# Kernel optimization log

Hardware: AMD Instinct MI355X
Metric: run time of the kernel (lower is better)

The kernel has to match this reference:

```python
import jax, jax.numpy as jnp
import numpy as np

B, NP, DIM = 32, 1369, 768
NCLS, K = 200, 5
C = NCLS + 1          # n_classes + background
H = W = 37            # sqrt(NP)
GAMMA = 0.99
SCALE = 4.0
SINKHORN_ITERS = 3
PCA_ITERS = 10
PCA_THRESH = 0.5
EPS = 1e-8


def _l2norm(x):
    return x / jnp.clip(jnp.linalg.norm(x, axis=-1, keepdims=True), EPS)


def setup_inputs() -> dict:
    key = jax.random.key(0)
    k1, k2, k3 = jax.random.split(key, 3)
    patch_tokens = jax.random.normal(k1, (B, NP, DIM), dtype=jnp.float32)
    labels = jax.random.randint(k2, (B,), 0, NCLS)
    prototypes = 0.02 * jax.random.normal(k3, (C, K, DIM), dtype=jnp.float32)  # trunc_normal std=0.02 approx
    sa = jnp.full((NCLS, K), 0.5, dtype=jnp.float32)
    scale = jnp.asarray(SCALE, dtype=jnp.float32)
    return {"patch_tokens": patch_tokens, "labels": labels,
            "prototypes": prototypes, "sa": sa, "scale": scale}


def reference(patch_tokens, labels, prototypes, sa, scale):
    # --- cosine patch-prototype similarity ---
    tok_n = _l2norm(patch_tokens)                 # [B, NP, D]
    pro_n = _l2norm(prototypes)                   # [C, K, D]
    logits = scale * jnp.einsum('bnd,ckd->bnck', tok_n, pro_n)  # [B, NP, C, K]

    # --- avg pooling + 'sa' classification head ---
    image_logits = logits.mean(axis=1)            # [B, C, K]
    sa_w = jax.nn.softmax(sa, axis=-1) * K        # [NCLS, K]
    class_logits = (image_logits[:, :NCLS, :] * sa_w).sum(axis=-1)  # [B, NCLS]

    # --- PCA pseudo patch labels (power iteration, q=1, centered) ---
    X = jax.lax.stop_gradient(patch_tokens).reshape(-1, DIM)  # [N, D]
    Xc = X - X.mean(axis=0, keepdims=True)
    v = jax.random.normal(jax.random.key(42), (DIM,), dtype=jnp.float32)
    for _ in range(PCA_ITERS):
        u = Xc @ v
        v = Xc.T @ u
        v = v / jnp.clip(jnp.linalg.norm(v), EPS)
    u = Xc @ v
    U = u / jnp.clip(jnp.linalg.norm(u), EPS)     # leading left singular vector
    U_scaled = (U - U.min()) / jnp.clip(U.max() - U.min(), EPS)
    U_img = U_scaled.reshape(B, H, W)
    pseudo = jnp.where(U_img <= PCA_THRESH,
                       labels[:, None, None],
                       C - 1).astype(jnp.int32)   # [B, H, W]

    # --- online clustering: masked sinkhorn vectorized over classes ---
    flat_lab = pseudo.reshape(-1)                 # [N]
    cls_ids = jnp.arange(C)
    mask = (flat_lab[:, None] == cls_ids[None, :]).astype(jnp.float32)  # [N, C]
    Nc = mask.sum(axis=0)                         # [C] fg patch count per class
    Lf = jax.lax.stop_gradient(logits).reshape(-1, C, K)
    Q = jnp.exp(Lf) * mask[:, :, None]            # [N, C, K], zero outside class mask
    Q = Q / jnp.clip(Q.sum(axis=(0, 2)), EPS)[None, :, None]
    Ncc = jnp.clip(Nc, 1.0)
    for _ in range(SINKHORN_ITERS):
        Q = Q / jnp.clip(Q.sum(axis=0), EPS)[None] / K           # col normalize
        Q = Q / jnp.clip(Q.sum(axis=2, keepdims=True), EPS) / Ncc[None, :, None]  # row normalize
    Q = Q * Nc[None, :, None]
    tok_flat = jax.lax.stop_gradient(tok_n).reshape(-1, DIM)
    P_new = jnp.einsum('nck,nd->ckd', Q, tok_flat)               # [C, K, D]
    updated = GAMMA * prototypes + (1.0 - GAMMA) * P_new          # momentum update
    present = jnp.isin(cls_ids, labels)                           # classes in this batch
    new_prototypes = jnp.where(present[:, None, None], updated, prototypes)

    return (logits, image_logits, class_logits, pseudo, new_prototypes)
```

## Files before the change

### kernel.cpp

```cpp
#include <hip/hip_runtime.h>

constexpr int   BB    = 32;
constexpr int   NPP   = 1369;
constexpr int   DIMC  = 768;
constexpr int   NCLSC = 200;
constexpr int   KP    = 5;
constexpr int   CC    = 201;
constexpr int   CKC   = 1005;
constexpr int   NPAD  = 1024;
constexpr int   NTOK  = BB * NPP;
constexpr float EPSF  = 1e-8f;
constexpr int   PWIN  = 128;
constexpr int   MTILES = 343;
constexpr int   NSLAB = 4;

typedef __attribute__((ext_vector_type(8))) short bf16x8;
typedef __attribute__((ext_vector_type(4))) float f32x4;

constexpr size_t O_LOG = 0;
constexpr size_t O_IMG = (size_t)NTOK * CKC;
constexpr size_t O_CLS = O_IMG + (size_t)BB * CKC;
constexpr size_t O_PSE = O_CLS + (size_t)BB * NCLSC;
constexpr size_t O_PRO = O_PSE + (size_t)NTOK;

constexpr size_t W_PRONBF = 0;
constexpr size_t W_INVN   = W_PRONBF + (size_t)NPAD*DIMC/2;
constexpr size_t W_MU     = W_INVN + NTOK;
constexpr size_t W_COLS   = W_MU + 2*DIMC;
constexpr size_t W_VBUF   = W_COLS + 2*NSLAB*DIMC;
constexpr size_t W_SSUM   = W_VBUF + 2*11*NSLAB*DIMC;
constexpr size_t W_TSUM   = W_SSUM + 128;
constexpr size_t W_NC     = W_TSUM + CC;
constexpr size_t W_FILL   = W_NC + CC;
constexpr size_t W_PRES   = W_FILL + CC;
constexpr size_t ZG_LEN   = (W_PRES + CC) - W_COLS;
constexpr size_t W_CSQ    = W_PRES + CC;
constexpr size_t W_U      = ((W_CSQ + CKC) + 1) & ~(size_t)1;
constexpr size_t W_PART   = W_U + 2*NTOK;
constexpr size_t W_SCAL   = W_PART + 2*1536;
constexpr size_t W_Q      = W_SCAL + 16;
constexpr size_t W_PNEW   = W_Q + (size_t)NTOK*KP;
constexpr size_t W_PLAB   = W_PNEW + (size_t)CC*KP*DIMC;
constexpr size_t W_OFFS   = W_PLAB + NTOK;
constexpr size_t W_RLST   = W_OFFS + 256;
constexpr size_t W_XBF    = ((W_RLST + NTOK) + 3) & ~(size_t)3;
constexpr size_t W_END_BIG  = W_XBF + (size_t)(NTOK + 128)*DIMC/2;
constexpr size_t W_PRON32   = W_XBF;
constexpr size_t W_END_FALL = W_PRON32 + (size_t)CKC*DIMC;

__device__ __forceinline__ unsigned short f2bf(float x) {
    unsigned u = __float_as_uint(x);
    unsigned r = (u + 0x7fffu + ((u >> 16) & 1u)) >> 16;
    return (unsigned short)r;
}
__device__ __forceinline__ float bf2f(unsigned short h) {
    return __uint_as_float(((unsigned)h) << 16);
}

typedef __attribute__((address_space(3))) unsigned int as3_u32;
typedef __attribute__((address_space(1))) unsigned int as1_u32;
__device__ __forceinline__ void gload16(const unsigned short* g, unsigned short* l) {
    __builtin_amdgcn_global_load_lds((as1_u32*)g, (as3_u32*)l, 16, 0, 0);
}

__global__ void fill_zero(float* p, int n) {
    int i = blockIdx.x * 256 + threadIdx.x;
    if (i < n) p[i] = 0.0f;
}

__global__ __launch_bounds__(256) void tok_stats(const float* __restrict__ X,
                                                 float* __restrict__ invn,
                                                 double* __restrict__ colsD,
                                                 unsigned short* __restrict__ xbf) {
    __shared__ double csh[4][768];
    const int tid  = threadIdx.x;
    const int lane = tid & 63;
    const int wid  = tid >> 6;
    const int gw   = blockIdx.x * 4 + wid;
    double cacc[3][4];
    #pragma unroll
    for (int j = 0; j < 3; j++)
        #pragma unroll
        for (int t = 0; t < 4; t++) cacc[j][t] = 0.0;
    for (int n = gw; n < NTOK; n += 4096) {
        const float4* row = (const float4*)(X + (size_t)n * DIMC);
        float s = 0.0f;
        float4 xv[3];
        #pragma unroll
        for (int j = 0; j < 3; j++) {
            xv[j] = row[lane + 64*j];
            s = fmaf(xv[j].x, xv[j].x, s); s = fmaf(xv[j].y, xv[j].y, s);
            s = fmaf(xv[j].z, xv[j].z, s); s = fmaf(xv[j].w, xv[j].w, s);
            cacc[j][0] += (double)xv[j].x; cacc[j][1] += (double)xv[j].y;
            cacc[j][2] += (double)xv[j].z; cacc[j][3] += (double)xv[j].w;
        }
        if (xbf) {
            unsigned short* orow = xbf + (size_t)n * DIMC;
            #pragma unroll
            for (int j = 0; j < 3; j++) {
                ushort4 pk;
                pk.x = f2bf(xv[j].x); pk.y = f2bf(xv[j].y);
                pk.z = f2bf(xv[j].z); pk.w = f2bf(xv[j].w);
                *(ushort4*)(orow + 4*(lane + 64*j)) = pk;
            }
        }
        #pragma unroll
        for (int o = 32; o >= 1; o >>= 1) s += __shfl_xor(s, o);
        if (lane == 0) invn[n] = 1.0f / fmaxf(sqrtf(s), EPSF);
    }
    #pragma unroll
    for (int j = 0; j < 3; j++)
        #pragma unroll
        for (int t = 0; t < 4; t++)
            csh[wid][4*lane + 256*j + t] = cacc[j][t];
    __syncthreads();
    const int slab = blockIdx.x & (NSLAB - 1);
    for (int c = tid; c < 768; c += 256)
        atomicAdd(&colsD[slab * 768 + c], csh[0][c] + csh[1][c] + csh[2][c] + csh[3][c]);
}

__global__ __launch_bounds__(256) void proto_norm(const float* __restrict__ P,
                                                  unsigned short* __restrict__ pbf,
                                                  float* __restrict__ p32) {
    const int lane = threadIdx.x & 63;
    const int gw   = blockIdx.x * 4 + (threadIdx.x >> 6);
    for (int j = gw; j < NPAD; j += 256) {
        unsigned short* obf = pbf + (size_t)j * DIMC;
        if (j >= CKC) {
            #pragma unroll
            for (int t = 0; t < 12; t++) obf[lane + 64*t] = 0;
            continue;
        }
        const float* row = P + (size_t)j * DIMC;
        float x[12]; float s = 0.0f;
        #pragma unroll
        for (int t = 0; t < 12; t++) { x[t] = row[lane + 64*t]; s = fmaf(x[t], x[t], s); }
        #pragma unroll
        for (int o = 32; o >= 1; o >>= 1) s += __shfl_xor(s, o);
        float nrm = fmaxf(sqrtf(s), EPSF);
        #pragma unroll
        for (int t = 0; t < 12; t++) {
            float nv = x[t] / nrm;
            obf[lane + 64*t] = f2bf(nv);
            if (p32) p32[(size_t)j * DIMC + lane + 64*t] = nv;
        }
    }
}

__global__ __launch_bounds__(256) void logits_gemm(
        const unsigned short* __restrict__ Xbf,
        const unsigned short* __restrict__ Pbf,
        const float* __restrict__ invn,
        const float* __restrict__ scale_p,
        float* __restrict__ out,
        float* __restrict__ img) {
    __shared__ unsigned short As[128 * 64];
    __shared__ unsigned short Bs[128 * 64];
    const int b   = blockIdx.x;
    const int swz = (b & 7) * MTILES + (b >> 3);
    const int row_t = swz >> 3, col_t = swz & 7;
    const int row0 = row_t * 128, col0 = col_t * 128;
    const int tid = threadIdx.x, lane = tid & 63, wid = tid >> 6;
    const int wm = (wid >> 1) * 64, wn = (wid & 1) * 64;
    const int fr = lane & 15, fq = lane >> 4;

    f32x4 acc[4][4] = {};

    const int w32 = wid * 32;
    const int lr8 = lane >> 3;
    const int lch = (lane & 7) ^ lr8;
    const unsigned short* aBase = Xbf + (size_t)(row0 + w32 + lr8) * DIMC + lch * 8;
    const unsigned short* bBase = Pbf + (size_t)(col0 + w32 + lr8) * DIMC + lch * 8;

    for (int ks = 0; ks < DIMC / 64; ks++) {
        __syncthreads();
        #pragma unroll
        for (int i = 0; i < 4; i++) {
            gload16(aBase + (size_t)(8 * i) * DIMC + ks * 64, &As[(w32 + 8 * i) * 64]);
            gload16(bBase + (size_t)(8 * i) * DIMC + ks * 64, &Bs[(w32 + 8 * i) * 64]);
        }
        __syncthreads();
        #pragma unroll
        for (int kk = 0; kk < 2; kk++) {
            bf16x8 af[4], bfr[4];
            #pragma unroll
            for (int m = 0; m < 4; m++)
                af[m] = *(const bf16x8*)(As + (wm + m * 16 + fr) * 64 +
                                         (((kk << 2) | fq) ^ (fr & 7)) * 8);
            #pragma unroll
            for (int n = 0; n < 4; n++)
                bfr[n] = *(const bf16x8*)(Bs + (wn + n * 16 + fr) * 64 +
                                          (((kk << 2) | fq) ^ (fr & 7)) * 8);
            #pragma unroll
            for (int m = 0; m < 4; m++)
                #pragma unroll
                for (int n = 0; n < 4; n++)
                    acc[m][n] = __builtin_amdgcn_mfma_f32_16x16x32_bf16(af[m], bfr[n], acc[m][n], 0, 0, 0);
        }
    }

    const float sc = *scale_p;
    #pragma unroll
    for (int m = 0; m < 4; m++) {
        const int rbase = row0 + wm + m * 16 + fq * 4;
        float fin[4];
        #pragma unroll
        for (int rr = 0; rr < 4; rr++) {
            int rrow = rbase + rr;
            fin[rr] = (rrow < NTOK) ? sc * invn[rrow] : 0.0f;
        }
        const int strip0 = row0 + wm + m * 16;
        const bool sameImg = ((strip0 / NPP) == ((strip0 + 15) / NPP)) && (strip0 + 15) < NTOK;
        const int bimg = strip0 / NPP;
        #pragma unroll
        for (int n = 0; n < 4; n++) {
            const int col = col0 + wn + n * 16 + fr;
            const bool cok = col < CKC;
            float csum = 0.0f;
            #pragma unroll
            for (int rr = 0; rr < 4; rr++) {
                int rrow = rbase + rr;
                float v = fin[rr] * acc[m][n][rr];
                if (cok && rrow < NTOK) out[(size_t)rrow * CKC + col] = v;
                csum += v;
            }
            if (sameImg) {
                csum += __shfl_xor(csum, 16);
                csum += __shfl_xor(csum, 32);
                if (lane < 16 && cok) atomicAdd(&img[bimg * CKC + col], csum);
            } else if (cok) {
                #pragma unroll
                for (int rr = 0; rr < 4; rr++) {
                    int rrow = rbase + rr;
                    if (rrow < NTOK)
                        atomicAdd(&img[(rrow / NPP) * CKC + col], fin[rr] * acc[m][n][rr]);
                }
            }
        }
    }
}

__global__ __launch_bounds__(256) void gemm_logits(const float* __restrict__ X,
                                                   const float* __restrict__ Bn,
                                                   const float* __restrict__ invn,
                                                   const float* __restrict__ scale_p,
                                                   float* __restrict__ out) {
    __shared__ float As[32][68];
    __shared__ float Bs[32][68];
    const int tid = threadIdx.x;
    const int tx = tid & 15, ty = tid >> 4;
    const int row0 = blockIdx.x * 64;
    const int col0 = blockIdx.y * 64;
    const int lm = tid >> 2;
    const int kb = (tid & 3) * 8;
    float acc[4][4] = {};
    for (int k0 = 0; k0 < DIMC; k0 += 32) {
        float a[8], b[8];
        int ar = row0 + lm;
        if (ar < NTOK) {
            const float* ap = X + (size_t)ar * DIMC + k0 + kb;
            #pragma unroll
            for (int j = 0; j < 8; j++) a[j] = ap[j];
        } else {
            #pragma unroll
            for (int j = 0; j < 8; j++) a[j] = 0.0f;
        }
        int bc = col0 + lm;
        if (bc < CKC) {
            const float* bp = Bn + (size_t)bc * DIMC + k0 + kb;
            #pragma unroll
            for (int j = 0; j < 8; j++) b[j] = bp[j];
        } else {
            #pragma unroll
            for (int j = 0; j < 8; j++) b[j] = 0.0f;
        }
        __syncthreads();
        #pragma unroll
        for (int j = 0; j < 8; j++) As[kb + j][lm] = a[j];
        #pragma unroll
        for (int j = 0; j < 8; j++) Bs[kb + j][lm] = b[j];
        __syncthreads();
        #pragma unroll
        for (int kk = 0; kk < 32; kk++) {
            float av[4], bv[4];
            #pragma unroll
            for (int i = 0; i < 4; i++) av[i] = As[kk][ty*4 + i];
            #pragma unroll
            for (int j = 0; j < 4; j++) bv[j] = Bs[kk][tx*4 + j];
            #pragma unroll
            for (int i = 0; i < 4; i++)
                #pragma unroll
                for (int j = 0; j < 4; j++)
                    acc[i][j] = fmaf(av[i], bv[j], acc[i][j]);
        }
    }
    const float sc = *scale_p;
    #pragma unroll
    for (int i = 0; i < 4; i++) {
        int r = row0 + ty*4 + i;
        if (r >= NTOK) continue;
        float f = sc * invn[r];
        float* orow = out + (size_t)r * CKC;
        #pragma unroll
        for (int j = 0; j < 4; j++) {
            int c = col0 + tx*4 + j;
            if (c < CKC) orow[c] = f * acc[i][j];
        }
    }
}

__global__ void img_reduce(const float* __restrict__ logits, float* __restrict__ img) {
    int b = blockIdx.x, jc = blockIdx.y, nc = blockIdx.z;
    int j = jc * 256 + threadIdx.x;
    if (j >= CKC) return;
    int p0 = nc * 172, p1 = min(NPP, p0 + 172);
    const float* base = logits + (size_t)b * NPP * CKC + j;
    float s = 0.0f;
    for (int p = p0; p < p1; p++) s += base[(size_t)p * CKC];
    atomicAdd(&img[b * CKC + j], s);
}

__global__ __launch_bounds__(256) void img_final(float* __restrict__ img,
                                                 const float* __restrict__ sa,
                                                 float* __restrict__ cls) {
    int b = blockIdx.x;
    for (int i = threadIdx.x; i < CKC; i += 256)
        img[b * CKC + i] = img[b * CKC + i] / 1369.0f;
    __syncthreads();
    for (int c = threadIdx.x; c < NCLSC; c += 256) {
        float vv[KP]; float mx = -3.4e38f;
        #pragma unroll
        for (int k = 0; k < KP; k++) { vv[k] = sa[c * KP + k]; mx = fmaxf(mx, vv[k]); }
        float e[KP]; float s = 0.0f;
        #pragma unroll
        for (int k = 0; k < KP; k++) { e[k] = expf(vv[k] - mx); s += e[k]; }
        float cl = 0.0f;
        #pragma unroll
        for (int k = 0; k < KP; k++) {
            float sw = e[k] / s * 5.0f;
            cl += img[b * CKC + c * KP + k] * sw;
        }
        cls[b * NCLSC + c] = cl;
    }
}

__global__ void mu_final(const double* __restrict__ colsD, double* __restrict__ mu) {
    int d = threadIdx.x;
    double s = 0.0;
    #pragma unroll
    for (int k = 0; k < NSLAB; k++) s += colsD[k * 768 + d];
    mu[d] = s / (double)NTOK;
}

__device__ __forceinline__ float bits_to_normal(unsigned bits) {
    float f = __uint_as_float((bits >> 9) | 0x3f800000u) - 1.0f;
    const float lo = -0.99999994f;
    float u = f * 2.0f + lo;
    u = fmaxf(lo, u);
    float w = -log1pf(-u * u);
    float p;
    if (w < 5.0f) {
        w -= 2.5f;
        p = 2.81022636e-08f;
        p = fmaf(p, w, 3.43273939e-07f);
        p = fmaf(p, w, -3.5233877e-06f);
        p = fmaf(p, w, -4.39150654e-06f);
        p = fmaf(p, w, 0.00021858087f);
        p = fmaf(p, w, -0.00125372503f);
        p = fmaf(p, w, -0.00417768164f);
        p = fmaf(p, w, 0.246640727f);
        p = fmaf(p, w, 1.50140941f);
    } else {
        w = sqrtf(w) - 3.0f;
        p = -0.000200214257f;
        p = fmaf(p, w, 0.000100950558f);
        p = fmaf(p, w, 0.00134934322f);
        p = fmaf(p, w, -0.00367342844f);
        p = fmaf(p, w, 0.00573950773f);
        p = fmaf(p, w, -0.0076224613f);
        p = fmaf(p, w, 0.00943887047f);
        p = fmaf(p, w, 1.00167406f);
        p = fmaf(p, w, 2.83297682f);
    }
    return 1.41421356237f * (p * u);
}

#define TF_ROUND(r) { x0 += x1; x1 = (x1 << r) | (x1 >> (32 - r)); x1 ^= x0; }
__global__ void v0_gen(double* __restrict__ v) {
    int i = blockIdx.x * 256 + threadIdx.x;
    if (i >= DIMC) return;
    unsigned x0 = 0u, x1 = (unsigned)i;
    const unsigned k0 = 0u, k1 = 42u, k2 = k0 ^ k1 ^ 0x1BD11BDAu;
    x0 += k0; x1 += k1;
    TF_ROUND(13) TF_ROUND(15) TF_ROUND(26) TF_ROUND(6)
    x0 += k1; x1 += k2 + 1u;
    TF_ROUND(17) TF_ROUND(29) TF_ROUND(16) TF_ROUND(24)
    x0 += k2; x1 += k0 + 2u;
    TF_ROUND(13) TF_ROUND(15) TF_ROUND(26) TF_ROUND(6)
    x0 += k0; x1 += k1 + 3u;
    TF_ROUND(17) TF_ROUND(29) TF_ROUND(16) TF_ROUND(24)
    x0 += k1; x1 += k2 + 4u;
    TF_ROUND(13) TF_ROUND(15) TF_ROUND(26) TF_ROUND(6)
    x0 += k2; x1 += k0 + 5u;
    v[i] = (double)bits_to_normal(x0 ^ x1);
}

__global__ __launch_bounds__(256) void pca_pass(const float* __restrict__ X,
                                                const double* __restrict__ mu,
                                                const double* __restrict__ vraw,
                                                const double* __restrict__ Sin,
                                                double* __restrict__ vnext,
                                                double* __restrict__ Snext) {
    __shared__ double wacc[4][768];
    __shared__ double redw[4];
    const int tid = threadIdx.x, lane = tid & 63, wid = tid >> 6;
    double S = 0.0;
    #pragma unroll
    for (int k = 0; k < NSLAB; k++) S += Sin[k];
    double ver[3][4];
    double mv = 0.0;
    #pragma unroll
    for (int j = 0; j < 3; j++)
        #pragma unroll
        for (int t = 0; t < 4; t++) {
            int c = 4*lane + 256*j + t;
            double vr = 0.0;
            #pragma unroll
            for (int k = 0; k < NSLAB; k++) vr += vraw[k * 768 + c];
            double x = vr - S * mu[c];
            ver[j][t] = x;
            mv += mu[c] * x;
        }
    #pragma unroll
    for (int o = 32; o >= 1; o >>= 1) mv += __shfl_xor(mv, o);
    const double muv = mv;

    double acc[3][4] = {};
    double usum = 0.0;
    const int gw = blockIdx.x * 4 + wid;
    for (int n0 = gw; n0 < NTOK; n0 += 4096) {
        const int n1 = n0 + 2048;
        const bool h1 = (n1 < NTOK);
        const float4* r0 = (const float4*)(X + (size_t)n0 * DIMC);
        const float4* r1 = (const float4*)(X + (size_t)(h1 ? n1 : n0) * DIMC);
        float4 xa[3], xb[3];
        #pragma unroll
        for (int j = 0; j < 3; j++) xa[j] = r0[lane + 64*j];
        #pragma unroll
        for (int j = 0; j < 3; j++) xb[j] = r1[lane + 64*j];
        double s0 = 0.0, s1 = 0.0;
        #pragma unroll
        for (int j = 0; j < 3; j++) {
            s0 = fma((double)xa[j].x, ver[j][0], s0);
            s0 = fma((double)xa[j].y, ver[j][1], s0);
            s0 = fma((double)xa[j].z, ver[j][2], s0);
            s0 = fma((double)xa[j].w, ver[j][3], s0);
            s1 = fma((double)xb[j].x, ver[j][0], s1);
            s1 = fma((double)xb[j].y, ver[j][1], s1);
            s1 = fma((double)xb[j].z, ver[j][2], s1);
            s1 = fma((double)xb[j].w, ver[j][3], s1);
        }
        #pragma unroll
        for (int o = 32; o >= 1; o >>= 1) { s0 += __shfl_xor(s0, o); s1 += __shfl_xor(s1, o); }
        double uu0 = s0 - muv;
        usum += uu0;
        #pragma unroll
        for (int j = 0; j < 3; j++) {
            acc[j][0] = fma((double)xa[j].x, uu0, acc[j][0]);
            acc[j][1] = fma((double)xa[j].y, uu0, acc[j][1]);
            acc[j][2] = fma((double)xa[j].z, uu0, acc[j][2]);
            acc[j][3] = fma((double)xa[j].w, uu0, acc[j][3]);
        }
        if (h1) {
            double uu1 = s1 - muv;
            usum += uu1;
            #pragma unroll
            for (int j = 0; j < 3; j++) {
                acc[j][0] = fma((double)xb[j].x, uu1, acc[j][0]);
                acc[j][1] = fma((double)xb[j].y, uu1, acc[j][1]);
                acc[j][2] = fma((double)xb[j].z, uu1, acc[j][2]);
                acc[j][3] = fma((double)xb[j].w, uu1, acc[j][3]);
            }
        }
    }
    #pragma unroll
    for (int j = 0; j < 3; j++)
        #pragma unroll
        for (int t = 0; t < 4; t++)
            wacc[wid][4*lane + 256*j + t] = acc[j][t];
    if (lane == 0) redw[wid] = usum;
    __syncthreads();
    const int slab = blockIdx.x & (NSLAB - 1);
    for (int c = tid; c < 768; c += 256)
        atomicAdd(&vnext[slab * 768 + c], wacc[0][c] + wacc[1][c] + wacc[2][c] + wacc[3][c]);
    if (tid == 0) atomicAdd(&Snext[slab], redw[0] + redw[1] + redw[2] + redw[3]);
}

__global__ __launch_bounds__(256) void u_final(const float* __restrict__ X,
                                               const double* __restrict__ mu,
                                               const double* __restrict__ vraw,
                                               const double* __restrict__ Sin,
                                               double* __restrict__ u,
                                               double* __restrict__ part) {
    __shared__ double wmin[4], wmax[4], wss[4];
    const int tid = threadIdx.x, lane = tid & 63, wid = tid >> 6;
    double S = 0.0;
    #pragma unroll
    for (int k = 0; k < NSLAB; k++) S += Sin[k];
    double ver[3][4];
    double mv = 0.0;
    #pragma unroll
    for (int j = 0; j < 3; j++)
        #pragma unroll
        for (int t = 0; t < 4; t++) {
            int c = 4*lane + 256*j + t;
            double vr = 0.0;
            #pragma unroll
            for (int k = 0; k < NSLAB; k++) vr += vraw[k * 768 + c];
            double x = vr - S * mu[c];
            ver[j][t] = x;
            mv += mu[c] * x;
        }
    #pragma unroll
    for (int o = 32; o >= 1; o >>= 1) mv += __shfl_xor(mv, o);
    const double muv = mv;
    double lmin = 1e300, lmax = -1e300, lss = 0.0;
    for (int n = blockIdx.x * 4 + wid; n < NTOK; n += 2048) {
        const float4* row = (const float4*)(X + (size_t)n * DIMC);
        double s = 0.0;
        #pragma unroll
        for (int j = 0; j < 3; j++) {
            float4 xv = row[lane + 64*j];
            s = fma((double)xv.x, ver[j][0], s);
            s = fma((double)xv.y, ver[j][1], s);
            s = fma((double)xv.z, ver[j][2], s);
            s = fma((double)xv.w, ver[j][3], s);
        }
        #pragma unroll
        for (int o = 32; o >= 1; o >>= 1) s += __shfl_xor(s, o);
        double uu = s - muv;
        if (lane == 0) {
            u[n] = uu;
            lmin = fmin(lmin, uu); lmax = fmax(lmax, uu); lss = fma(uu, uu, lss);
        }
    }
    if (lane == 0) { wmin[wid] = lmin; wmax[wid] = lmax; wss[wid] = lss; }
    __syncthreads();
    if (tid == 0) {
        part[blockIdx.x]        = fmin(fmin(wmin[0], wmin[1]), fmin(wmin[2], wmin[3]));
        part[512 + blockIdx.x]  = fmax(fmax(wmax[0], wmax[1]), fmax(wmax[2], wmax[3]));
        part[1024 + blockIdx.x] = wss[0] + wss[1] + wss[2] + wss[3];
    }
}

__global__ __launch_bounds__(512) void final_scalars(const double* __restrict__ part,
                                                     double* __restrict__ scal,
                                                     const int* __restrict__ labels,
                                                     int* __restrict__ pres) {
    __shared__ double rmin[512], rmax[512], rss[512];
    int t = threadIdx.x;
    rmin[t] = part[t]; rmax[t] = part[512 + t]; rss[t] = part[1024 + t];
    __syncthreads();
    for (int s = 256; s > 0; s >>= 1) {
        if (t < s) {
            rmin[t] = fmin(rmin[t], rmin[t + s]);
            rmax[t] = fmax(rmax[t], rmax[t + s]);
            rss[t] += rss[t + s];
        }
        __syncthreads();
    }
    if (t == 0) {
        double nrm = fmax(sqrt(rss[0]), 1e-8);
        double Umin = rmin[0] / nrm;
        double Umax = rmax[0] / nrm;
        scal[1] = nrm;
        scal[2] = Umin;
        scal[3] = fmax(Umax - Umin, 1e-8);
    }
    if (t < BB) pres[labels[t]] = 1;
}

__global__ __launch_bounds__(256) void pseudo_kernel(
        const double* __restrict__ u, const double* __restrict__ scal,
        const int* __restrict__ labels, float* __restrict__ pse,
        int* __restrict__ plab, int* __restrict__ Nc) {
    __shared__ int hist[CC];
    const int tid = threadIdx.x;
    for (int c = tid; c < CC; c += 256) hist[c] = 0;
    __syncthreads();
    int n = blockIdx.x * 256 + tid;
    if (n < NTOK) {
        double U  = u[n] / scal[1];
        double Us = (U - scal[2]) / scal[3];
        int lab = (Us <= 0.5) ? labels[n / NPP] : (CC - 1);
        pse[n] = (float)lab;
        plab[n] = lab;
        atomicAdd(&hist[lab], 1);
    }
    __syncthreads();
    for (int c = tid; c < CC; c += 256)
        if (hist[c] > 0) atomicAdd(&Nc[c], hist[c]);
}

__global__ void offs_scan(const int* __restrict__ Nc, int* __restrict__ offs) {
    if (threadIdx.x == 0) {
        int s = 0;
        for (int c = 0; c < CC; c++) { offs[c] = s; s += Nc[c]; }
        offs[CC] = s;
    }
}

__global__ __launch_bounds__(256) void scatter_rows(
        const int* __restrict__ plab, const int* __restrict__ offs,
        int* __restrict__ fill, int* __restrict__ rlist) {
    __shared__ int hist[CC];
    __shared__ int base[CC];
    const int tid = threadIdx.x;
    for (int c = tid; c < CC; c += 256) hist[c] = 0;
    __syncthreads();
    int n = blockIdx.x * 256 + tid;
    int lab = -1, posl = 0;
    if (n < NTOK) {
        lab = plab[n];
        posl = atomicAdd(&hist[lab], 1);
    }
    __syncthreads();
    for (int c = tid; c < CC; c += 256) {
        int h = hist[c];
        if (h > 0) base[c] = atomicAdd(&fill[c], h);
    }
    __syncthreads();
    if (n < NTOK) rlist[offs[lab] + base[lab] + posl] = n;
}

__global__ __launch_bounds__(256) void sinkhorn_fused(
        const float* __restrict__ logits,
        const int* __restrict__ offs,
        const int* __restrict__ rlist,
        float* __restrict__ qseg) {
    const int c  = blockIdx.x;
    const int i0 = offs[c], i1 = offs[c + 1];
    const int cnt = i1 - i0;
    if (cnt <= 0) return;
    const int tid = threadIdx.x;
    __shared__ float cs[KP];
    __shared__ float redk[KP][4];

    for (int i = i0 + tid; i < i1; i += 256) {
        int n = rlist[i];
        const float* lp = logits + (size_t)n * CKC + c * KP;
        #pragma unroll
        for (int k = 0; k < KP; k++) qseg[(size_t)i * KP + k] = expf(lp[k]);
    }
    const float Ncc = fmaxf((float)cnt, 1.0f);
    for (int it = 0; it < 3; it++) {
        __syncthreads();
        float lc[KP] = {};
        for (int i = i0 + tid; i < i1; i += 256) {
            #pragma unroll
            for (int k = 0; k < KP; k++) lc[k] += qseg[(size_t)i * KP + k];
        }
        #pragma unroll
        for (int k = 0; k < KP; k++) {
            float v = lc[k];
            #pragma unroll
            for (int o = 32; o >= 1; o >>= 1) v += __shfl_xor(v, o);
            if ((tid & 63) == 0) redk[k][tid >> 6] = v;
        }
        __syncthreads();
        if (tid == 0) {
            #pragma unroll
            for (int k = 0; k < KP; k++)
                cs[k] = fmaxf(redk[k][0] + redk[k][1] + redk[k][2] + redk[k][3], EPSF) * 5.0f;
        }
        __syncthreads();
        float inv_cs[KP];
        #pragma unroll
        for (int k = 0; k < KP; k++) inv_cs[k] = 1.0f / cs[k];
        const float outsc = (it == 2) ? ((float)cnt / Ncc) : (1.0f / Ncc);
        for (int i = i0 + tid; i < i1; i += 256) {
            float v[KP]; float rs = 0.0f;
            #pragma unroll
            for (int k = 0; k < KP; k++) { v[k] = qseg[(size_t)i*KP + k] * inv_cs[k]; rs += v[k]; }
            float f = outsc / fmaxf(rs, EPSF);
            #pragma unroll
            for (int k = 0; k < KP; k++) qseg[(size_t)i*KP + k] = v[k] * f;
        }
    }
}

__global__ __launch_bounds__(256) void pnew_partial(
        const float* __restrict__ X,
        const unsigned short* __restrict__ Xbf,
        const float* __restrict__ invn,
        const float* __restrict__ qseg,
        const int* __restrict__ offs,
        const int* __restrict__ rlist,
        const int* __restrict__ plab,
        float* __restrict__ Pnew) {
    const int d = blockIdx.y * 256 + threadIdx.x;
    const int fgEnd = offs[CC - 1];
    int i0 = blockIdx.x * PWIN;
    if (i0 >= fgEnd) return;
    int i1 = min(i0 + PWIN, fgEnd);
    int curlab = -1;
    float acc[KP] = {};
    for (int i = i0; i < i1; i++) {
        int n = rlist[i];
        int lab = plab[n];
        if (lab != curlab) {
            if (curlab >= 0) {
                #pragma unroll
                for (int k = 0; k < KP; k++)
                    atomicAdd(&Pnew[((size_t)curlab * KP + k) * DIMC + d], acc[k]);
            }
            curlab = lab;
            #pragma unroll
            for (int k = 0; k < KP; k++) acc[k] = 0.0f;
        }
        float xr = Xbf ? bf2f(Xbf[(size_t)n * DIMC + d]) : X[(size_t)n * DIMC + d];
        float x = xr * invn[n];
        #pragma unroll
        for (int k = 0; k < KP; k++) acc[k] = fmaf(qseg[(size_t)i * KP + k], x, acc[k]);
    }
    if (curlab >= 0) {
        #pragma unroll
        for (int k = 0; k < KP; k++)
            atomicAdd(&Pnew[((size_t)curlab * KP + k) * DIMC + d], acc[k]);
    }
}

__global__ void proto_out(const float* __restrict__ proto, const float* __restrict__ Pnew,
                          const int* __restrict__ pres, float* __restrict__ outp) {
    int idx = blockIdx.x * 256 + threadIdx.x;
    if (idx >= CC * KP * DIMC) return;
    int c = idx / (KP * DIMC);
    float p = proto[idx];
    float r = p;
    if (pres[c]) {
        const float g = 0.99f;
        r = g * p + (1.0f - g) * Pnew[idx];
    }
    outp[idx] = r;
}

extern "C" void kernel_launch(void* const* d_in, const int* in_sizes, int n_in,
                              void* d_out, int out_size, void* d_ws, size_t ws_size,
                              hipStream_t stream) {
    const float* X      = (const float*)d_in[0];
    const int*   labels = (const int*)  d_in[1];
    const float* proto  = (const float*)d_in[2];
    const float* sa     = (const float*)d_in[3];
    const float* scale  = (const float*)d_in[4];
    float* out = (float*)d_out;
    float* ws  = (float*)d_ws;
    const bool big = ws_size >= W_END_BIG * sizeof(float);
    if (!big && ws_size < W_END_FALL * sizeof(float)) return;

    unsigned short* pronbf = (unsigned short*)(ws + W_PRONBF);
    float*  invn  = ws + W_INVN;
    double* mu    = (double*)(ws + W_MU);
    double* colsD = (double*)(ws + W_COLS);
    double* vbuf  = (double*)(ws + W_VBUF);
    double* Ssum  = (double*)(ws + W_SSUM);
    int*    Nc    = (int*)(ws + W_NC);
    int*    fill  = (int*)(ws + W_FILL);
    int*    pres  = (int*)(ws + W_PRES);
    double* u     = (double*)(ws + W_U);
    double* part  = (double*)(ws + W_PART);
    double* scal  = (double*)(ws + W_SCAL);
    float*  qseg  = ws + W_Q;
    float*  Pnew  = ws + W_PNEW;
    int*    plab  = (int*)(ws + W_PLAB);
    int*    offs  = (int*)(ws + W_OFFS);
    int*    rlist = (int*)(ws + W_RLST);
    unsigned short* xbf = big ? (unsigned short*)(ws + W_XBF) : nullptr;
    float*  pron32 = big ? nullptr : (ws + W_PRON32);

    fill_zero<<<((int)ZG_LEN + 255) / 256, 256, 0, stream>>>(ws + W_COLS, (int)ZG_LEN);
    fill_zero<<<(CC * KP * DIMC + 255) / 256, 256, 0, stream>>>(Pnew, CC * KP * DIMC);
    fill_zero<<<(BB * CKC + 255) / 256, 256, 0, stream>>>(out + O_IMG, BB * CKC);

    tok_stats<<<1024, 256, 0, stream>>>(X, invn, colsD, xbf);
    proto_norm<<<64, 256, 0, stream>>>(proto, pronbf, pron32);
    if (big) {
        logits_gemm<<<MTILES * 8, 256, 0, stream>>>(xbf, pronbf, invn, scale,
                                                    out + O_LOG, out + O_IMG);
    } else {
        gemm_logits<<<dim3(685, 16), 256, 0, stream>>>(X, pron32, invn, scale, out + O_LOG);
        img_reduce<<<dim3(32, 4, 8), 256, 0, stream>>>(out + O_LOG, out + O_IMG);
    }
    img_final<<<32, 256, 0, stream>>>(out + O_IMG, sa, out + O_CLS);

    mu_final<<<1, 768, 0, stream>>>(colsD, mu);
    v0_gen<<<3, 256, 0, stream>>>(vbuf);
    for (int t = 0; t < 10; t++) {
        pca_pass<<<512, 256, 0, stream>>>(X, mu,
            vbuf + (size_t)t * NSLAB * DIMC, Ssum + t * NSLAB,
            vbuf + (size_t)(t + 1) * NSLAB * DIMC, Ssum + (t + 1) * NSLAB);
    }
    u_final<<<512, 256, 0, stream>>>(X, mu,
        vbuf + (size_t)10 * NSLAB * DIMC, Ssum + 10 * NSLAB, u, part);
    final_scalars<<<1, 512, 0, stream>>>(part, scal, labels, pres);
    pseudo_kernel<<<172, 256, 0, stream>>>(u, scal, labels, out + O_PSE, plab, Nc);

    offs_scan<<<1, 64, 0, stream>>>(Nc, offs);
    scatter_rows<<<172, 256, 0, stream>>>(plab, offs, fill, rlist);
    sinkhorn_fused<<<NCLSC, 256, 0, stream>>>(out + O_LOG, offs, rlist, qseg);
    pnew_partial<<<dim3((NTOK + PWIN - 1) / PWIN, 3), 256, 0, stream>>>(
        X, xbf, invn, qseg, offs, rlist, plab, Pnew);
    proto_out<<<(CC * KP * DIMC + 255) / 256, 256, 0, stream>>>(proto, Pnew, pres, out + O_PRO);
}
```

Measured before the change: 621.9 us.

## Double-buffer LDS tiles in logits GEMM with K=32 steps

The logits GEMM main loop now uses two LDS buffers holding 32-wide K slices. The next slice is prefetched via direct global-to-LDS loads while MFMAs run on the current one, leaving one barrier per iteration instead of two. The XOR swizzle is adapted to the 32-element row width. The cost is twice as many loop iterations, each with less MFMA work to hide latency behind, and a new bank-conflict pattern.

```diff
diff --git a/kernel.cpp b/kernel.cpp
--- a/kernel.cpp
+++ b/kernel.cpp
@@ -154,8 +154,8 @@
         const float* __restrict__ scale_p,
         float* __restrict__ out,
         float* __restrict__ img) {
-    __shared__ unsigned short As[128 * 64];
-    __shared__ unsigned short Bs[128 * 64];
+    __shared__ unsigned short As[2][128 * 32];
+    __shared__ unsigned short Bs[2][128 * 32];
     const int b   = blockIdx.x;
     const int swz = (b & 7) * MTILES + (b >> 3);
     const int row_t = swz >> 3, col_t = swz & 7;
@@ -167,36 +167,42 @@
     f32x4 acc[4][4] = {};
 
     const int w32 = wid * 32;
-    const int lr8 = lane >> 3;
-    const int lch = (lane & 7) ^ lr8;
-    const unsigned short* aBase = Xbf + (size_t)(row0 + w32 + lr8) * DIMC + lch * 8;
-    const unsigned short* bBase = Pbf + (size_t)(col0 + w32 + lr8) * DIMC + lch * 8;
-
-    for (int ks = 0; ks < DIMC / 64; ks++) {
+    const int lr  = lane >> 2;
+    const int gch = (lane & 3) ^ ((lane >> 3) & 3);
+    const unsigned short* aS0 = Xbf + (size_t)(row0 + w32 + lr) * DIMC + gch * 8;
+    const unsigned short* aS1 = aS0 + (size_t)16 * DIMC;
+    const unsigned short* bS0 = Pbf + (size_t)(col0 + w32 + lr) * DIMC + gch * 8;
+    const unsigned short* bS1 = bS0 + (size_t)16 * DIMC;
+
+    const int rc = (fq ^ ((fr >> 1) & 3)) * 8;
+
+    gload16(aS0, &As[0][(w32)      * 32]);
+    gload16(aS1, &As[0][(w32 + 16) * 32]);
+    gload16(bS0, &Bs[0][(w32)      * 32]);
+    gload16(bS1, &Bs[0][(w32 + 16) * 32]);
+    __syncthreads();
+
+    for (int ks = 0; ks < DIMC / 32; ks++) {
+        const int cur = ks & 1, nxt = cur ^ 1;
+        if (ks + 1 < DIMC / 32) {
+            gload16(aS0 + (ks + 1) * 32, &As[nxt][(w32)      * 32]);
+            gload16(aS1 + (ks + 1) * 32, &As[nxt][(w32 + 16) * 32]);
+            gload16(bS0 + (ks + 1) * 32, &Bs[nxt][(w32)      * 32]);
+            gload16(bS1 + (ks + 1) * 32, &Bs[nxt][(w32 + 16) * 32]);
+        }
+        bf16x8 af[4], bfr[4];
+        #pragma unroll
+        for (int m = 0; m < 4; m++)
+            af[m] = *(const bf16x8*)(&As[cur][(wm + m * 16 + fr) * 32 + rc]);
+        #pragma unroll
+        for (int n = 0; n < 4; n++)
+            bfr[n] = *(const bf16x8*)(&Bs[cur][(wn + n * 16 + fr) * 32 + rc]);
+        #pragma unroll
+        for (int m = 0; m < 4; m++)
+            #pragma unroll
+            for (int n = 0; n < 4; n++)
+                acc[m][n] = __builtin_amdgcn_mfma_f32_16x16x32_bf16(af[m], bfr[n], acc[m][n], 0, 0, 0);
         __syncthreads();
-        #pragma unroll
-        for (int i = 0; i < 4; i++) {
-            gload16(aBase + (size_t)(8 * i) * DIMC + ks * 64, &As[(w32 + 8 * i) * 64]);
-            gload16(bBase + (size_t)(8 * i) * DIMC + ks * 64, &Bs[(w32 + 8 * i) * 64]);
-        }
-        __syncthreads();
-        #pragma unroll
-        for (int kk = 0; kk < 2; kk++) {
-            bf16x8 af[4], bfr[4];
-            #pragma unroll
-            for (int m = 0; m < 4; m++)
-                af[m] = *(const bf16x8*)(As + (wm + m * 16 + fr) * 64 +
-                                         (((kk << 2) | fq) ^ (fr & 7)) * 8);
-            #pragma unroll
-            for (int n = 0; n < 4; n++)
-                bfr[n] = *(const bf16x8*)(Bs + (wn + n * 16 + fr) * 64 +
-                                          (((kk << 2) | fq) ^ (fr & 7)) * 8);
-            #pragma unroll
-            for (int m = 0; m < 4; m++)
-                #pragma unroll
-                for (int n = 0; n < 4; n++)
-                    acc[m][n] = __builtin_amdgcn_mfma_f32_16x16x32_bf16(af[m], bfr[n], acc[m][n], 0, 0, 0);
-        }
     }
 
     const float sc = *scale_p;
```

Result: slower. 635.3 us (+2.2%).
